# Optimization experiments

Hardware: AMD Instinct MI355X
Metric: run time of the kernel (lower is better)

## Reference

```python
import jax, jax.numpy as jnp
import numpy as np
from jax import lax

B, T, N, D = 64, 2048, 64, 128


def setup_inputs() -> dict:
    key = jax.random.key(0)
    k0, k1, k2, k3, k4 = jax.random.split(key, 5)
    return {
        "X": jax.random.normal(k0, (B, T, D), dtype=jnp.float32),
        "transition_matrix": jax.random.uniform(k1, (N, N), dtype=jnp.float32) / N,
        "state_priors": jax.random.uniform(k2, (N,), dtype=jnp.float32) / N,
        "means": jax.random.normal(k3, (N, D), dtype=jnp.float32),
        "log_vars": jax.random.normal(k4, (N, D), dtype=jnp.float32) * 0.1,
    }


def _emission_logprobs(X, means, log_vars):
    # Diagonal-Gaussian log density per state, vectorized over (B,T,N).
    # sum_d (x-mu)^2 / var expanded into GEMMs to avoid a (B,T,N,D) tensor.
    inv_var = jnp.exp(-log_vars)                               # (N,D)
    t1 = jnp.einsum('btd,nd->btn', X * X, inv_var)             # sum x^2/var
    t2 = jnp.einsum('btd,nd->btn', X, means * inv_var)         # sum x*mu/var
    t3 = jnp.sum(means * means * inv_var + log_vars, axis=-1)  # (N,)
    d = X.shape[-1]
    log2pi = jnp.log(jnp.asarray(2.0 * np.pi, dtype=X.dtype))
    return -0.5 * (t1 - 2.0 * t2 + t3 + d * log2pi)            # (B,T,N)


def reference(X, transition_matrix, state_priors, means, log_vars):
    log_A = jax.nn.log_softmax(transition_matrix, axis=1)      # (N,N)
    log_pi = jax.nn.log_softmax(state_priors, axis=0)          # (N,)
    log_b = _emission_logprobs(X, means, log_vars)             # (B,T,N)

    alpha0 = log_pi + log_b[:, 0]                              # (B,N)
    lb_rest = jnp.moveaxis(log_b[:, 1:], 1, 0)                 # (T-1,B,N)

    def step(alpha_prev, lb_t):
        # alpha_t[j] = log_b_t[j] + logsumexp_i(alpha_{t-1}[i] + log_A[i,j])
        scores = alpha_prev[:, :, None] + log_A[None, :, :]    # (B,N,N)
        alpha_t = lb_t + jax.scipy.special.logsumexp(scores, axis=1)
        return alpha_t, None

    alpha_T, _ = lax.scan(step, alpha0, lb_rest)
    # original gathers log-sum at the last timestep, then sums over subjects
    return jnp.sum(jax.scipy.special.logsumexp(alpha_T, axis=-1))
```

## Files before the change

### kernel.cpp

```cpp
#include <hip/hip_runtime.h>


constexpr int ATF_OFF  = 0;
constexpr int PI_OFF   = 2048;
constexpr int CN_OFF   = 2112;
constexpr int WBF_OFF  = 2176;
constexpr int MV_OFF   = 10368;
constexpr int PART_OFF = 141440;
constexpr int GLS_OFF  = 141504;
constexpr int E_OFF    = 145600;
constexpr int G_OFF    = 4339904;

typedef __attribute__((ext_vector_type(8))) short bf16x8;
typedef __attribute__((ext_vector_type(16))) float f32x16;

union BU { unsigned u[4]; bf16x8 v; };

__device__ inline float wave_max(float v) {
  #pragma unroll
  for (int off = 1; off < 64; off <<= 1) v = fmaxf(v, __shfl_xor(v, off));
  return v;
}
__device__ inline float wave_sum(float v) {
  #pragma unroll
  for (int off = 1; off < 64; off <<= 1) v += __shfl_xor(v, off);
  return v;
}
__device__ inline float read_lane(float v, int l) {
  return __uint_as_float(__builtin_amdgcn_readlane(__float_as_uint(v), l));
}
__device__ inline unsigned f2bf(float f) {
  unsigned u = __float_as_uint(f);
  u += 0x7FFFu + ((u >> 16) & 1u);
  return u >> 16;
}
__device__ inline unsigned cvt_pk(float lo, float hi) {
  unsigned r;
  asm("v_cvt_pk_bf16_f32 %0, %1, %2" : "=v"(r) : "v"(lo), "v"(hi));
  return r;
}

__global__ void setup_kernel(const float* __restrict__ trans,
                             const float* __restrict__ priors,
                             const float* __restrict__ means,
                             const float* __restrict__ log_vars,
                             float* __restrict__ ws) {
  __shared__ float Psh[64 * 64];
  int tid = threadIdx.x, blk = blockIdx.x;

  if (blk == 0) {
    int lane = tid & 63, w = tid >> 6;
    for (int r = 0; r < 16; ++r) {
      int i = w * 16 + r;
      float x = trans[i * 64 + lane];
      float m = wave_max(x);
      float s = wave_sum(__expf(x - m));
      Psh[i * 64 + lane] = __expf(x - (m + __logf(s)));
    }
    if (w == 0) {
      float x = priors[lane];
      float m = wave_max(x);
      float s = wave_sum(__expf(x - m));
      ws[PI_OFF + lane] = __expf(x - (m + __logf(s)));
    }
    __syncthreads();
    for (int idx = tid; idx < 512; idx += 256) {
      int f = idx >> 6, l = idx & 63;
      int I = f >> 2, Kb = f & 3;
      int m = 32 * I + (l & 31);
      int kb = 16 * Kb + 8 * (l >> 5);
      unsigned u[4];
      #pragma unroll
      for (int p = 0; p < 4; ++p) {
        unsigned a = f2bf(Psh[(kb + 2 * p) * 64 + m]);
        unsigned b = f2bf(Psh[(kb + 2 * p + 1) * 64 + m]);
        u[p] = a | (b << 16);
      }
      *reinterpret_cast<uint4*>(&ws[ATF_OFF + idx * 4]) = make_uint4(u[0], u[1], u[2], u[3]);
    }
  } else if (blk <= 8) {
    int idx = (blk - 1) * 256 + tid;
    int f = idx >> 6, l = idx & 63;
    int Kb = f >> 1, J = f & 1;
    int n = 32 * J + (l & 31);
    int kb = 16 * Kb + 8 * (l >> 5);
    unsigned u[4];
    #pragma unroll
    for (int p = 0; p < 4; ++p) {
      int k0 = kb + 2 * p, k1 = k0 + 1;
      int d0 = k0 & 127, d1 = k1 & 127;
      float iv0 = __expf(-log_vars[n * 128 + d0]);
      float iv1 = __expf(-log_vars[n * 128 + d1]);
      float a  = (k0 < 128) ? (-0.5f * iv0) : (means[n * 128 + d0] * iv0);
      float bb = (k1 < 128) ? (-0.5f * iv1) : (means[n * 128 + d1] * iv1);
      u[p] = f2bf(a) | (f2bf(bb) << 16);
    }
    *reinterpret_cast<uint4*>(&ws[WBF_OFF + idx * 4]) = make_uint4(u[0], u[1], u[2], u[3]);
  } else {
    float* part = Psh;
    int n = tid & 63, g = tid >> 6;
    float s = 0.f;
    for (int d = 32 * g; d < 32 * g + 32; ++d) {
      float lv = log_vars[n * 128 + d];
      float mu = means[n * 128 + d];
      s += mu * mu * __expf(-lv) + lv;
    }
    part[g * 64 + n] = s;
    __syncthreads();
    if (tid < 64) {
      float tot = (part[tid] + part[64 + tid]) + (part[128 + tid] + part[192 + tid]);
      ws[CN_OFF + tid] = -0.5f * (tot + 128.0f * 1.8378770664093453f);
    }
  }
}

__global__ __launch_bounds__(256) void emis_kernel(const float* __restrict__ X,
                                                   float* __restrict__ ws) {
  __shared__ uint4 WBs[2048];
  int tid = threadIdx.x;
  const uint4* wbf = reinterpret_cast<const uint4*>(&ws[WBF_OFF]);
  #pragma unroll
  for (int i = 0; i < 8; ++i) WBs[tid + 256 * i] = wbf[tid + 256 * i];

  int lane = tid & 63, w = tid >> 6;
  int il = lane & 31, h = lane >> 5;
  size_t row = (size_t)blockIdx.x * 128 + w * 32 + il;
  const float* Xr = X + row * 128;

  bf16x8 ax[8], asq[8];
  #pragma unroll
  for (int s = 0; s < 8; ++s) {
    float4 v0 = *reinterpret_cast<const float4*>(Xr + s * 16 + 8 * h);
    float4 v1 = *reinterpret_cast<const float4*>(Xr + s * 16 + 8 * h + 4);
    BU bx, bq;
    bx.u[0] = cvt_pk(v0.x, v0.y); bx.u[1] = cvt_pk(v0.z, v0.w);
    bx.u[2] = cvt_pk(v1.x, v1.y); bx.u[3] = cvt_pk(v1.z, v1.w);
    bq.u[0] = cvt_pk(v0.x * v0.x, v0.y * v0.y);
    bq.u[1] = cvt_pk(v0.z * v0.z, v0.w * v0.w);
    bq.u[2] = cvt_pk(v1.x * v1.x, v1.y * v1.y);
    bq.u[3] = cvt_pk(v1.z * v1.z, v1.w * v1.w);
    ax[s] = bx.v; asq[s] = bq.v;
  }
  __syncthreads();

  f32x16 acc0, acc1;
  #pragma unroll
  for (int z = 0; z < 16; ++z) { acc0[z] = 0.f; acc1[z] = 0.f; }
  #pragma unroll
  for (int Kb = 0; Kb < 8; ++Kb) {
    bf16x8 b0 = reinterpret_cast<const BU*>(&WBs[(2 * Kb + 0) * 64 + lane])->v;
    bf16x8 b1 = reinterpret_cast<const BU*>(&WBs[(2 * Kb + 1) * 64 + lane])->v;
    acc0 = __builtin_amdgcn_mfma_f32_32x32x16_bf16(asq[Kb], b0, acc0, 0, 0, 0);
    acc1 = __builtin_amdgcn_mfma_f32_32x32x16_bf16(asq[Kb], b1, acc1, 0, 0, 0);
  }
  #pragma unroll
  for (int Kb = 8; Kb < 16; ++Kb) {
    bf16x8 b0 = reinterpret_cast<const BU*>(&WBs[(2 * Kb + 0) * 64 + lane])->v;
    bf16x8 b1 = reinterpret_cast<const BU*>(&WBs[(2 * Kb + 1) * 64 + lane])->v;
    acc0 = __builtin_amdgcn_mfma_f32_32x32x16_bf16(ax[Kb - 8], b0, acc0, 0, 0, 0);
    acc1 = __builtin_amdgcn_mfma_f32_32x32x16_bf16(ax[Kb - 8], b1, acc1, 0, 0, 0);
  }

  float cn0 = ws[CN_OFF + il];
  float cn1 = ws[CN_OFF + 32 + il];
  unsigned short* Ep = reinterpret_cast<unsigned short*>(&ws[E_OFF]);
  float* MVp = &ws[MV_OFF];
  size_t tbase = (size_t)blockIdx.x * 128 + w * 32;
  #pragma unroll
  for (int e = 0; e < 16; ++e) {
    float v0 = acc0[e] + cn0;
    float v1 = acc1[e] + cn1;
    float mx = fmaxf(v0, v1);
    #pragma unroll
    for (int off = 1; off < 32; off <<= 1) mx = fmaxf(mx, __shfl_xor(mx, off));
    int r = (e & 3) + 8 * (e >> 2) + 4 * h;
    size_t t = tbase + r;
    Ep[t * 64 + il]      = (unsigned short)f2bf(__expf(v0 - mx));
    Ep[t * 64 + 32 + il] = (unsigned short)f2bf(__expf(v1 - mx));
    if (il == 0) MVp[t] = mx;
  }
}

__global__ __launch_bounds__(128, 4) void fwd1_scan(float* __restrict__ ws) {
  const int tid = threadIdx.x;
  const int lane = tid & 63, J = tid >> 6;
  const int h = lane >> 5, il = lane & 31;
  const int job = blockIdx.x, b = job >> 5, cch = job & 31;

  bf16x8 atf0, atf1, atf2, atf3, atf4, atf5, atf6, atf7;
  atf0 = *reinterpret_cast<const bf16x8*>(&ws[ATF_OFF + (0 * 64 + lane) * 4]);
  atf1 = *reinterpret_cast<const bf16x8*>(&ws[ATF_OFF + (1 * 64 + lane) * 4]);
  atf2 = *reinterpret_cast<const bf16x8*>(&ws[ATF_OFF + (2 * 64 + lane) * 4]);
  atf3 = *reinterpret_cast<const bf16x8*>(&ws[ATF_OFF + (3 * 64 + lane) * 4]);
  atf4 = *reinterpret_cast<const bf16x8*>(&ws[ATF_OFF + (4 * 64 + lane) * 4]);
  atf5 = *reinterpret_cast<const bf16x8*>(&ws[ATF_OFF + (5 * 64 + lane) * 4]);
  atf6 = *reinterpret_cast<const bf16x8*>(&ws[ATF_OFF + (6 * 64 + lane) * 4]);
  atf7 = *reinterpret_cast<const bf16x8*>(&ws[ATF_OFF + (7 * 64 + lane) * 4]);

  bf16x8 bf0, bf1, bf2, bf3;
  {
    int js0 = 32 * J + il - 8 * h;
#define IDF(dst, Kb) { int js = js0 - 16 * (Kb); BU bu_;                      \
    _Pragma("unroll")                                                         \
    for (int p = 0; p < 4; ++p)                                               \
      bu_.u[p] = ((js >> 1) == p) ? ((js & 1) ? 0x3F800000u : 0x00003F80u) : 0u; \
    dst = bu_.v; }
    IDF(bf0, 0) IDF(bf1, 1) IDF(bf2, 2) IDF(bf3, 3)
#undef IDF
  }

  const int tstart = 1 + cch * 64;
  const int len = (cch == 31) ? 63 : 64;
  const char* Eb = (const char*)(ws + E_OFF) + ((size_t)b * 2048 + tstart) * 128;

  float Ls = 0.0f;

#define LOADE(dst, idx) {                                                     \
    const char* Ep_ = Eb + (size_t)(idx) * 128;                               \
    _Pragma("unroll")                                                         \
    for (int q_ = 0; q_ < 4; ++q_) {                                          \
      dst[q_]     = *reinterpret_cast<const uint2*>(Ep_ + 16 * q_ + 8 * h);   \
      dst[4 + q_] = *reinterpret_cast<const uint2*>(Ep_ + 64 + 16 * q_ + 8 * h); \
    } }

#define SX(W, z, I)                                                           \
  ({ uint2 u_ = W[4 * (I) + ((z) >> 2)];                                      \
     unsigned w_ = (((z) >> 1) & 1) ? u_.y : u_.x;                            \
     __uint_as_float(((z) & 1) ? (w_ & 0xFFFF0000u) : (w_ << 16)); })

#define BBS(dst, At, p, I, W) {                                               \
    unsigned xe0 = cvt_pk((At)[8*(p)+0] * SX(W, 8*(p)+0, I),                  \
                          (At)[8*(p)+1] * SX(W, 8*(p)+1, I));                 \
    unsigned xe1 = cvt_pk((At)[8*(p)+2] * SX(W, 8*(p)+2, I),                  \
                          (At)[8*(p)+3] * SX(W, 8*(p)+3, I));                 \
    unsigned xo0 = cvt_pk((At)[8*(p)+4] * SX(W, 8*(p)+4, I),                  \
                          (At)[8*(p)+5] * SX(W, 8*(p)+5, I));                 \
    unsigned xo1 = cvt_pk((At)[8*(p)+6] * SX(W, 8*(p)+6, I),                  \
                          (At)[8*(p)+7] * SX(W, 8*(p)+7, I));                 \
    asm("v_permlane32_swap_b32 %0, %1" : "+v"(xe0), "+v"(xo0));               \
    asm("v_permlane32_swap_b32 %0, %1" : "+v"(xe1), "+v"(xo1));               \
    BU bu_; bu_.u[0] = xe0; bu_.u[1] = xe1; bu_.u[2] = xo0; bu_.u[3] = xo1;   \
    dst = bu_.v; }

#define MFMA_HEAD(d, A, B)                                                    \
    asm("v_mfma_f32_32x32x16_bf16 %0, %1, %2, 0"                              \
        : "=&v"(d) : "v"(A), "v"(B));
#define MFMA_ACC(d, A, B)                                                     \
    asm("v_mfma_f32_32x32x16_bf16 %0, %1, %2, %0"                             \
        : "+v"(d) : "v"(A), "v"(B));

#define STEP(EW, DO_RN) {                                                     \
    f32x16 a0, a1;                                                            \
    MFMA_HEAD(a0, atf0, bf0)                                                  \
    MFMA_HEAD(a1, atf4, bf0)                                                  \
    MFMA_ACC(a0, atf1, bf1)                                                   \
    MFMA_ACC(a1, atf5, bf1)                                                   \
    MFMA_ACC(a0, atf2, bf2)                                                   \
    MFMA_ACC(a1, atf6, bf2)                                                   \
    MFMA_ACC(a0, atf3, bf3)                                                   \
    MFMA_ACC(a1, atf7, bf3)                                                   \
    asm volatile("s_nop 7\n\ts_nop 7\n\ts_nop 3" : "+v"(a0), "+v"(a1));       \
    if (DO_RN) {                                                              \
      float mx = 0.f;                                                         \
      _Pragma("unroll")                                                       \
      for (int z = 0; z < 16; ++z) mx = fmaxf(mx, fmaxf(a0[z], a1[z]));       \
      mx = wave_max(mx);                                                      \
      float inv = 1.0f / mx;                                                  \
      Ls += __logf(mx);                                                       \
      _Pragma("unroll")                                                       \
      for (int z = 0; z < 16; ++z) { a0[z] *= inv; a1[z] *= inv; }            \
    }                                                                         \
    BBS(bf0, a0, 0, 0, EW) BBS(bf1, a0, 1, 0, EW)                             \
    BBS(bf2, a1, 0, 1, EW) BBS(bf3, a1, 1, 1, EW) }

  uint2 eA[8];
  #pragma unroll 1
  for (int step = 0; step < len; ++step) {
    LOADE(eA, step);
    STEP(eA, ((step & 7) == 7));
  }

#undef STEP
#undef MFMA_ACC
#undef MFMA_HEAD
#undef BBS
#undef SX
#undef LOADE

  unsigned short* Gb = reinterpret_cast<unsigned short*>(&ws[G_OFF]) + (size_t)job * 4096;
#define GST(fr, Kb) { BU bu_; bu_.v = fr;                                     \
    _Pragma("unroll")                                                         \
    for (int p = 0; p < 4; ++p) {                                             \
      int k = 16 * (Kb) + 8 * h + 2 * p;                                      \
      Gb[k * 64 + 32 * J + il]       = (unsigned short)(bu_.u[p] & 0xFFFFu);  \
      Gb[(k + 1) * 64 + 32 * J + il] = (unsigned short)(bu_.u[p] >> 16);      \
    } }
  GST(bf0, 0) GST(bf1, 1) GST(bf2, 2) GST(bf3, 3)
#undef GST
  if (lane == 0) ws[GLS_OFF + job * 2 + J] = Ls;
}

__global__ __launch_bounds__(64, 1) void fwd2_combine(float* __restrict__ ws) {
  int b = blockIdx.x, j = threadIdx.x;

  float Ms = 0.f;
  for (int k = 0; k < 32; ++k) Ms += ws[MV_OFF + (size_t)b * 2048 + k * 64 + j];
  Ms = wave_sum(Ms);

  const unsigned short* E0 =
      reinterpret_cast<const unsigned short*>(&ws[E_OFF]) + (size_t)b * 2048 * 64;
  float w = ws[PI_OFF + j] * __uint_as_float(((unsigned)E0[j]) << 16);
  float Lacc = Ms;

  const unsigned short* Gb =
      reinterpret_cast<const unsigned short*>(&ws[G_OFF]) + (size_t)b * 32 * 4096;
  for (int c = 0; c < 32; ++c) {
    const uint4* gp = reinterpret_cast<const uint4*>(Gb + (size_t)c * 4096 + j * 64);
    uint4 gw[8];
    #pragma unroll
    for (int s = 0; s < 8; ++s) gw[s] = gp[s];
    float gv[64];
    #pragma unroll
    for (int s = 0; s < 8; ++s) {
      gv[8 * s + 0] = __uint_as_float(gw[s].x << 16);
      gv[8 * s + 1] = __uint_as_float(gw[s].x & 0xFFFF0000u);
      gv[8 * s + 2] = __uint_as_float(gw[s].y << 16);
      gv[8 * s + 3] = __uint_as_float(gw[s].y & 0xFFFF0000u);
      gv[8 * s + 4] = __uint_as_float(gw[s].z << 16);
      gv[8 * s + 5] = __uint_as_float(gw[s].z & 0xFFFF0000u);
      gv[8 * s + 6] = __uint_as_float(gw[s].w << 16);
      gv[8 * s + 7] = __uint_as_float(gw[s].w & 0xFFFF0000u);
    }
    float l0 = 0.f, l1 = 0.f, h0 = 0.f, h1 = 0.f;
    #pragma unroll
    for (int i = 0; i < 32; i += 2) {
      l0 = fmaf(read_lane(w, i + 0), gv[i + 0], l0);
      l1 = fmaf(read_lane(w, i + 1), gv[i + 1], l1);
      h0 = fmaf(read_lane(w, 32 + i + 0), gv[32 + i + 0], h0);
      h1 = fmaf(read_lane(w, 32 + i + 1), gv[32 + i + 1], h1);
    }
    float ylo = l0 + l1, yhi = h0 + h1;
    float g0 = ws[GLS_OFF + (b * 32 + c) * 2 + 0];
    float g1 = ws[GLS_OFF + (b * 32 + c) * 2 + 1];
    float Lm = fmaxf(g0, g1);
    float y = __expf(g0 - Lm) * ylo + __expf(g1 - Lm) * yhi;
    float s = wave_sum(y);
    w = y * (1.0f / s);
    Lacc += Lm + __logf(s);
  }
  float S = wave_sum(w);
  if (j == 0) ws[PART_OFF + b] = Lacc + __logf(S);
}

__global__ void final_kernel(const float* __restrict__ part, float* __restrict__ out) {
  float v = part[threadIdx.x];
  float s = wave_sum(v);
  if (threadIdx.x == 0) out[0] = s;
}

extern "C" void kernel_launch(void* const* d_in, const int* in_sizes, int n_in,
                              void* d_out, int out_size, void* d_ws, size_t ws_size,
                              hipStream_t stream) {
  const float* X        = (const float*)d_in[0];
  const float* trans    = (const float*)d_in[1];
  const float* priors   = (const float*)d_in[2];
  const float* means    = (const float*)d_in[3];
  const float* log_vars = (const float*)d_in[4];
  float* ws  = (float*)d_ws;
  float* out = (float*)d_out;

  hipLaunchKernelGGL(setup_kernel, dim3(10), dim3(256), 0, stream,
                     trans, priors, means, log_vars, ws);
  hipLaunchKernelGGL(emis_kernel, dim3(1024), dim3(256), 0, stream, X, ws);
  hipLaunchKernelGGL(fwd1_scan, dim3(2048), dim3(128), 0, stream, ws);
  hipLaunchKernelGGL(fwd2_combine, dim3(64), dim3(64), 0, stream, ws);
  hipLaunchKernelGGL(final_kernel, dim3(1), dim3(64), 0, stream,
                     ws + PART_OFF, out);
}
```

Measured before the change: 138.7 us.

## Interleave two independent scan chunks per block to hide MFMA latency

Each block of the chunked forward scan now processes two independent time chunks, interleaving their MFMA chains, normalisation and emission loads. The MFMA dependency latency of one chunk can then overlap with the conversion and scaling work of the other. The grid is halved and the occupancy hint drops from 4 to 2 blocks to make room for the doubled register state. The last chunk with 63 steps is handled by clamping the load index and skipping its final finish step.

```diff
diff --git a/kernel.cpp b/kernel.cpp
--- a/kernel.cpp
+++ b/kernel.cpp
@@ -181,11 +181,13 @@
   }
 }
 
-__global__ __launch_bounds__(128, 4) void fwd1_scan(float* __restrict__ ws) {
+__global__ __launch_bounds__(128, 2) void fwd1_scan(float* __restrict__ ws) {
   const int tid = threadIdx.x;
   const int lane = tid & 63, J = tid >> 6;
   const int h = lane >> 5, il = lane & 31;
-  const int job = blockIdx.x, b = job >> 5, cch = job & 31;
+  const int jobA = blockIdx.x * 2, jobB = jobA + 1;
+  const int b = jobA >> 5;
+  const int cchA = jobA & 31, cchB = jobB & 31;
 
   bf16x8 atf0, atf1, atf2, atf3, atf4, atf5, atf6, atf7;
   atf0 = *reinterpret_cast<const bf16x8*>(&ws[ATF_OFF + (0 * 64 + lane) * 4]);
@@ -197,7 +199,7 @@
   atf6 = *reinterpret_cast<const bf16x8*>(&ws[ATF_OFF + (6 * 64 + lane) * 4]);
   atf7 = *reinterpret_cast<const bf16x8*>(&ws[ATF_OFF + (7 * 64 + lane) * 4]);
 
-  bf16x8 bf0, bf1, bf2, bf3;
+  bf16x8 bfA0, bfA1, bfA2, bfA3, bfB0, bfB1, bfB2, bfB3;
   {
     int js0 = 32 * J + il - 8 * h;
 #define IDF(dst, Kb) { int js = js0 - 16 * (Kb); BU bu_;                      \
@@ -205,18 +207,19 @@
     for (int p = 0; p < 4; ++p)                                               \
       bu_.u[p] = ((js >> 1) == p) ? ((js & 1) ? 0x3F800000u : 0x00003F80u) : 0u; \
     dst = bu_.v; }
-    IDF(bf0, 0) IDF(bf1, 1) IDF(bf2, 2) IDF(bf3, 3)
+    IDF(bfA0, 0) IDF(bfA1, 1) IDF(bfA2, 2) IDF(bfA3, 3)
+    IDF(bfB0, 0) IDF(bfB1, 1) IDF(bfB2, 2) IDF(bfB3, 3)
 #undef IDF
   }
 
-  const int tstart = 1 + cch * 64;
-  const int len = (cch == 31) ? 63 : 64;
-  const char* Eb = (const char*)(ws + E_OFF) + ((size_t)b * 2048 + tstart) * 128;
-
-  float Ls = 0.0f;
-
-#define LOADE(dst, idx) {                                                     \
-    const char* Ep_ = Eb + (size_t)(idx) * 128;                               \
+  const int lenB = (cchB == 31) ? 63 : 64;
+  const char* EbA = (const char*)(ws + E_OFF) + ((size_t)b * 2048 + 1 + cchA * 64) * 128;
+  const char* EbB = (const char*)(ws + E_OFF) + ((size_t)b * 2048 + 1 + cchB * 64) * 128;
+
+  float LsA = 0.0f, LsB = 0.0f;
+
+#define LOADE(dst, base, idx) {                                               \
+    const char* Ep_ = (base) + (size_t)(idx) * 128;                           \
     _Pragma("unroll")                                                         \
     for (int q_ = 0; q_ < 4; ++q_) {                                          \
       dst[q_]     = *reinterpret_cast<const uint2*>(Ep_ + 16 * q_ + 8 * h);   \
@@ -249,16 +252,17 @@
     asm("v_mfma_f32_32x32x16_bf16 %0, %1, %2, %0"                             \
         : "+v"(d) : "v"(A), "v"(B));
 
-#define STEP(EW, DO_RN) {                                                     \
-    f32x16 a0, a1;                                                            \
-    MFMA_HEAD(a0, atf0, bf0)                                                  \
-    MFMA_HEAD(a1, atf4, bf0)                                                  \
-    MFMA_ACC(a0, atf1, bf1)                                                   \
-    MFMA_ACC(a1, atf5, bf1)                                                   \
-    MFMA_ACC(a0, atf2, bf2)                                                   \
-    MFMA_ACC(a1, atf6, bf2)                                                   \
-    MFMA_ACC(a0, atf3, bf3)                                                   \
-    MFMA_ACC(a1, atf7, bf3)                                                   \
+#define MFMA8(a0, a1, b0, b1, b2, b3) {                                       \
+    MFMA_HEAD(a0, atf0, b0)                                                   \
+    MFMA_HEAD(a1, atf4, b0)                                                   \
+    MFMA_ACC(a0, atf1, b1)                                                    \
+    MFMA_ACC(a1, atf5, b1)                                                    \
+    MFMA_ACC(a0, atf2, b2)                                                    \
+    MFMA_ACC(a1, atf6, b2)                                                    \
+    MFMA_ACC(a0, atf3, b3)                                                    \
+    MFMA_ACC(a1, atf7, b3) }
+
+#define FINISH(a0, a1, b0, b1, b2, b3, EW, DO_RN, Ls) {                       \
     asm volatile("s_nop 7\n\ts_nop 7\n\ts_nop 3" : "+v"(a0), "+v"(a1));       \
     if (DO_RN) {                                                              \
       float mx = 0.f;                                                         \
@@ -270,24 +274,42 @@
       _Pragma("unroll")                                                       \
       for (int z = 0; z < 16; ++z) { a0[z] *= inv; a1[z] *= inv; }            \
     }                                                                         \
-    BBS(bf0, a0, 0, 0, EW) BBS(bf1, a0, 1, 0, EW)                             \
-    BBS(bf2, a1, 0, 1, EW) BBS(bf3, a1, 1, 1, EW) }
-
-  uint2 eA[8];
+    BBS(b0, a0, 0, 0, EW) BBS(b1, a0, 1, 0, EW)                               \
+    BBS(b2, a1, 0, 1, EW) BBS(b3, a1, 1, 1, EW) }
+
+  uint2 eA[8], eB[8];
+  LOADE(eA, EbA, 0);
+  LOADE(eB, EbB, 0);
+
+  f32x16 aA0, aA1, aB0, aB1;
+  MFMA8(aA0, aA1, bfA0, bfA1, bfA2, bfA3)
+  MFMA8(aB0, aB1, bfB0, bfB1, bfB2, bfB3)
+
   #pragma unroll 1
-  for (int step = 0; step < len; ++step) {
-    LOADE(eA, step);
-    STEP(eA, ((step & 7) == 7));
-  }
-
-#undef STEP
+  for (int s = 0; s < 63; ++s) {
+    bool rn = ((s & 7) == 7);
+    FINISH(aA0, aA1, bfA0, bfA1, bfA2, bfA3, eA, rn, LsA)
+    LOADE(eA, EbA, s + 1)
+    MFMA8(aA0, aA1, bfA0, bfA1, bfA2, bfA3)
+    FINISH(aB0, aB1, bfB0, bfB1, bfB2, bfB3, eB, rn, LsB)
+    LOADE(eB, EbB, (s + 1 < lenB) ? (s + 1) : (lenB - 1))
+    MFMA8(aB0, aB1, bfB0, bfB1, bfB2, bfB3)
+  }
+  FINISH(aA0, aA1, bfA0, bfA1, bfA2, bfA3, eA, true, LsA)
+  if (lenB == 64) {
+    FINISH(aB0, aB1, bfB0, bfB1, bfB2, bfB3, eB, true, LsB)
+  }
+
+#undef FINISH
+#undef MFMA8
 #undef MFMA_ACC
 #undef MFMA_HEAD
 #undef BBS
 #undef SX
 #undef LOADE
 
-  unsigned short* Gb = reinterpret_cast<unsigned short*>(&ws[G_OFF]) + (size_t)job * 4096;
+  {
+    unsigned short* Gb = reinterpret_cast<unsigned short*>(&ws[G_OFF]) + (size_t)jobA * 4096;
 #define GST(fr, Kb) { BU bu_; bu_.v = fr;                                     \
     _Pragma("unroll")                                                         \
     for (int p = 0; p < 4; ++p) {                                             \
@@ -295,9 +317,15 @@
       Gb[k * 64 + 32 * J + il]       = (unsigned short)(bu_.u[p] & 0xFFFFu);  \
       Gb[(k + 1) * 64 + 32 * J + il] = (unsigned short)(bu_.u[p] >> 16);      \
     } }
-  GST(bf0, 0) GST(bf1, 1) GST(bf2, 2) GST(bf3, 3)
+    GST(bfA0, 0) GST(bfA1, 1) GST(bfA2, 2) GST(bfA3, 3)
+    Gb += 4096;
+    GST(bfB0, 0) GST(bfB1, 1) GST(bfB2, 2) GST(bfB3, 3)
 #undef GST
-  if (lane == 0) ws[GLS_OFF + job * 2 + J] = Ls;
+  }
+  if (lane == 0) {
+    ws[GLS_OFF + jobA * 2 + J] = LsA;
+    ws[GLS_OFF + jobB * 2 + J] = LsB;
+  }
 }
 
 __global__ __launch_bounds__(64, 1) void fwd2_combine(float* __restrict__ ws) {
@@ -372,7 +400,7 @@
   hipLaunchKernelGGL(setup_kernel, dim3(10), dim3(256), 0, stream,
                      trans, priors, means, log_vars, ws);
   hipLaunchKernelGGL(emis_kernel, dim3(1024), dim3(256), 0, stream, X, ws);
-  hipLaunchKernelGGL(fwd1_scan, dim3(2048), dim3(128), 0, stream, ws);
+  hipLaunchKernelGGL(fwd1_scan, dim3(1024), dim3(128), 0, stream, ws);
   hipLaunchKernelGGL(fwd2_combine, dim3(64), dim3(64), 0, stream, ws);
   hipLaunchKernelGGL(final_kernel, dim3(1), dim3(64), 0, stream,
                      ws + PART_OFF, out);
```

Result: slower. 145.6 us (+5.0%).

## Fuse emission GEMM into chunked scan kernel, keep emissions in LDS

Applied to the files above, without the earlier changes.

The separate emission kernel goes away. Each scan block now computes the emission probabilities for its own 64-timestep chunk with MFMA and stores them as bf16 in shared memory, so the 16 MB emission tensor no longer round-trips through global memory. The t=0 emission is written to a small fp32 global slot for the combine kernel to read. The combine kernel also prefetches the next chunk's transfer matrix while computing the current one. In exchange, every block reloads the weight fragments from global memory instead of from shared memory, and the GEMM work is spread over 128-thread blocks.

```diff
diff --git a/kernel.cpp b/kernel.cpp
--- a/kernel.cpp
+++ b/kernel.cpp
@@ -8,8 +8,8 @@
 constexpr int MV_OFF   = 10368;
 constexpr int PART_OFF = 141440;
 constexpr int GLS_OFF  = 141504;
-constexpr int E_OFF    = 145600;
-constexpr int G_OFF    = 4339904;
+constexpr int E0G_OFF  = 145600;
+constexpr int G_OFF    = 149696;
 
 typedef __attribute__((ext_vector_type(8))) short bf16x8;
 typedef __attribute__((ext_vector_type(16))) float f32x16;
@@ -114,78 +114,83 @@
   }
 }
 
-__global__ __launch_bounds__(256) void emis_kernel(const float* __restrict__ X,
-                                                   float* __restrict__ ws) {
-  __shared__ uint4 WBs[2048];
-  int tid = threadIdx.x;
-  const uint4* wbf = reinterpret_cast<const uint4*>(&ws[WBF_OFF]);
-  #pragma unroll
-  for (int i = 0; i < 8; ++i) WBs[tid + 256 * i] = wbf[tid + 256 * i];
-
-  int lane = tid & 63, w = tid >> 6;
-  int il = lane & 31, h = lane >> 5;
-  size_t row = (size_t)blockIdx.x * 128 + w * 32 + il;
-  const float* Xr = X + row * 128;
-
-  bf16x8 ax[8], asq[8];
-  #pragma unroll
-  for (int s = 0; s < 8; ++s) {
-    float4 v0 = *reinterpret_cast<const float4*>(Xr + s * 16 + 8 * h);
-    float4 v1 = *reinterpret_cast<const float4*>(Xr + s * 16 + 8 * h + 4);
-    BU bx, bq;
-    bx.u[0] = cvt_pk(v0.x, v0.y); bx.u[1] = cvt_pk(v0.z, v0.w);
-    bx.u[2] = cvt_pk(v1.x, v1.y); bx.u[3] = cvt_pk(v1.z, v1.w);
-    bq.u[0] = cvt_pk(v0.x * v0.x, v0.y * v0.y);
-    bq.u[1] = cvt_pk(v0.z * v0.z, v0.w * v0.w);
-    bq.u[2] = cvt_pk(v1.x * v1.x, v1.y * v1.y);
-    bq.u[3] = cvt_pk(v1.z * v1.z, v1.w * v1.w);
-    ax[s] = bx.v; asq[s] = bq.v;
-  }
-  __syncthreads();
-
-  f32x16 acc0, acc1;
-  #pragma unroll
-  for (int z = 0; z < 16; ++z) { acc0[z] = 0.f; acc1[z] = 0.f; }
-  #pragma unroll
-  for (int Kb = 0; Kb < 8; ++Kb) {
-    bf16x8 b0 = reinterpret_cast<const BU*>(&WBs[(2 * Kb + 0) * 64 + lane])->v;
-    bf16x8 b1 = reinterpret_cast<const BU*>(&WBs[(2 * Kb + 1) * 64 + lane])->v;
-    acc0 = __builtin_amdgcn_mfma_f32_32x32x16_bf16(asq[Kb], b0, acc0, 0, 0, 0);
-    acc1 = __builtin_amdgcn_mfma_f32_32x32x16_bf16(asq[Kb], b1, acc1, 0, 0, 0);
-  }
-  #pragma unroll
-  for (int Kb = 8; Kb < 16; ++Kb) {
-    bf16x8 b0 = reinterpret_cast<const BU*>(&WBs[(2 * Kb + 0) * 64 + lane])->v;
-    bf16x8 b1 = reinterpret_cast<const BU*>(&WBs[(2 * Kb + 1) * 64 + lane])->v;
-    acc0 = __builtin_amdgcn_mfma_f32_32x32x16_bf16(ax[Kb - 8], b0, acc0, 0, 0, 0);
-    acc1 = __builtin_amdgcn_mfma_f32_32x32x16_bf16(ax[Kb - 8], b1, acc1, 0, 0, 0);
-  }
-
-  float cn0 = ws[CN_OFF + il];
-  float cn1 = ws[CN_OFF + 32 + il];
-  unsigned short* Ep = reinterpret_cast<unsigned short*>(&ws[E_OFF]);
-  float* MVp = &ws[MV_OFF];
-  size_t tbase = (size_t)blockIdx.x * 128 + w * 32;
-  #pragma unroll
-  for (int e = 0; e < 16; ++e) {
-    float v0 = acc0[e] + cn0;
-    float v1 = acc1[e] + cn1;
-    float mx = fmaxf(v0, v1);
-    #pragma unroll
-    for (int off = 1; off < 32; off <<= 1) mx = fmaxf(mx, __shfl_xor(mx, off));
-    int r = (e & 3) + 8 * (e >> 2) + 4 * h;
-    size_t t = tbase + r;
-    Ep[t * 64 + il]      = (unsigned short)f2bf(__expf(v0 - mx));
-    Ep[t * 64 + 32 + il] = (unsigned short)f2bf(__expf(v1 - mx));
-    if (il == 0) MVp[t] = mx;
-  }
-}
-
-__global__ __launch_bounds__(128, 4) void fwd1_scan(float* __restrict__ ws) {
+__global__ __launch_bounds__(128, 4) void fused_scan(const float* __restrict__ X,
+                                                     float* __restrict__ ws) {
+  __shared__ __align__(16) unsigned short Esh[64 * 64];
+
   const int tid = threadIdx.x;
   const int lane = tid & 63, J = tid >> 6;
   const int h = lane >> 5, il = lane & 31;
   const int job = blockIdx.x, b = job >> 5, cch = job & 31;
+  const int tstart = 1 + cch * 64;
+  const int len = (cch == 31) ? 63 : 64;
+
+  {
+    int i_lane = J * 32 + il;
+    int t_lane = tstart + i_lane;
+    if (cch == 31 && i_lane == 63) t_lane = 0;
+    const float* Xr = X + ((size_t)b * 2048 + t_lane) * 128;
+
+    bf16x8 ax[8], asq[8];
+    #pragma unroll
+    for (int s = 0; s < 8; ++s) {
+      float4 v0 = *reinterpret_cast<const float4*>(Xr + s * 16 + 8 * h);
+      float4 v1 = *reinterpret_cast<const float4*>(Xr + s * 16 + 8 * h + 4);
+      BU bx, bq;
+      bx.u[0] = cvt_pk(v0.x, v0.y); bx.u[1] = cvt_pk(v0.z, v0.w);
+      bx.u[2] = cvt_pk(v1.x, v1.y); bx.u[3] = cvt_pk(v1.z, v1.w);
+      bq.u[0] = cvt_pk(v0.x * v0.x, v0.y * v0.y);
+      bq.u[1] = cvt_pk(v0.z * v0.z, v0.w * v0.w);
+      bq.u[2] = cvt_pk(v1.x * v1.x, v1.y * v1.y);
+      bq.u[3] = cvt_pk(v1.z * v1.z, v1.w * v1.w);
+      ax[s] = bx.v; asq[s] = bq.v;
+    }
+
+    const uint4* wbf = reinterpret_cast<const uint4*>(&ws[WBF_OFF]);
+    f32x16 acc0, acc1;
+    #pragma unroll
+    for (int z = 0; z < 16; ++z) { acc0[z] = 0.f; acc1[z] = 0.f; }
+    #pragma unroll
+    for (int Kb = 0; Kb < 8; ++Kb) {
+      BU b0, b1;
+      *reinterpret_cast<uint4*>(b0.u) = wbf[(2 * Kb + 0) * 64 + lane];
+      *reinterpret_cast<uint4*>(b1.u) = wbf[(2 * Kb + 1) * 64 + lane];
+      acc0 = __builtin_amdgcn_mfma_f32_32x32x16_bf16(asq[Kb], b0.v, acc0, 0, 0, 0);
+      acc1 = __builtin_amdgcn_mfma_f32_32x32x16_bf16(asq[Kb], b1.v, acc1, 0, 0, 0);
+    }
+    #pragma unroll
+    for (int Kb = 8; Kb < 16; ++Kb) {
+      BU b0, b1;
+      *reinterpret_cast<uint4*>(b0.u) = wbf[(2 * Kb + 0) * 64 + lane];
+      *reinterpret_cast<uint4*>(b1.u) = wbf[(2 * Kb + 1) * 64 + lane];
+      acc0 = __builtin_amdgcn_mfma_f32_32x32x16_bf16(ax[Kb - 8], b0.v, acc0, 0, 0, 0);
+      acc1 = __builtin_amdgcn_mfma_f32_32x32x16_bf16(ax[Kb - 8], b1.v, acc1, 0, 0, 0);
+    }
+
+    float cn0 = ws[CN_OFF + il];
+    float cn1 = ws[CN_OFF + 32 + il];
+    float* MVp = &ws[MV_OFF] + (size_t)b * 2048;
+    #pragma unroll
+    for (int e = 0; e < 16; ++e) {
+      float v0 = acc0[e] + cn0;
+      float v1 = acc1[e] + cn1;
+      float mx = fmaxf(v0, v1);
+      #pragma unroll
+      for (int off = 1; off < 32; off <<= 1) mx = fmaxf(mx, __shfl_xor(mx, off));
+      int r = 32 * J + (e & 3) + 8 * (e >> 2) + 4 * h;
+      float e0 = __expf(v0 - mx), e1 = __expf(v1 - mx);
+      if (cch == 31 && r == 63) {
+        ws[E0G_OFF + b * 64 + il]      = e0;
+        ws[E0G_OFF + b * 64 + 32 + il] = e1;
+        if (il == 0) MVp[0] = mx;
+      } else {
+        Esh[r * 64 + il]      = (unsigned short)f2bf(e0);
+        Esh[r * 64 + 32 + il] = (unsigned short)f2bf(e1);
+        if (il == 0) MVp[tstart + r] = mx;
+      }
+    }
+  }
+  __syncthreads();
 
   bf16x8 atf0, atf1, atf2, atf3, atf4, atf5, atf6, atf7;
   atf0 = *reinterpret_cast<const bf16x8*>(&ws[ATF_OFF + (0 * 64 + lane) * 4]);
@@ -209,14 +214,10 @@
 #undef IDF
   }
 
-  const int tstart = 1 + cch * 64;
-  const int len = (cch == 31) ? 63 : 64;
-  const char* Eb = (const char*)(ws + E_OFF) + ((size_t)b * 2048 + tstart) * 128;
-
   float Ls = 0.0f;
 
 #define LOADE(dst, idx) {                                                     \
-    const char* Ep_ = Eb + (size_t)(idx) * 128;                               \
+    const char* Ep_ = reinterpret_cast<const char*>(Esh) + (size_t)(idx) * 128; \
     _Pragma("unroll")                                                         \
     for (int q_ = 0; q_ < 4; ++q_) {                                          \
       dst[q_]     = *reinterpret_cast<const uint2*>(Ep_ + 16 * q_ + 8 * h);   \
@@ -307,18 +308,23 @@
   for (int k = 0; k < 32; ++k) Ms += ws[MV_OFF + (size_t)b * 2048 + k * 64 + j];
   Ms = wave_sum(Ms);
 
-  const unsigned short* E0 =
-      reinterpret_cast<const unsigned short*>(&ws[E_OFF]) + (size_t)b * 2048 * 64;
-  float w = ws[PI_OFF + j] * __uint_as_float(((unsigned)E0[j]) << 16);
+  float w = ws[PI_OFF + j] * ws[E0G_OFF + b * 64 + j];
   float Lacc = Ms;
 
   const unsigned short* Gb =
       reinterpret_cast<const unsigned short*>(&ws[G_OFF]) + (size_t)b * 32 * 4096;
+  const uint4* gbase = reinterpret_cast<const uint4*>(Gb);
+
+  uint4 gw[8];
+  #pragma unroll
+  for (int s = 0; s < 8; ++s) gw[s] = gbase[j * 4 + s];
+
   for (int c = 0; c < 32; ++c) {
-    const uint4* gp = reinterpret_cast<const uint4*>(Gb + (size_t)c * 4096 + j * 64);
-    uint4 gw[8];
-    #pragma unroll
-    for (int s = 0; s < 8; ++s) gw[s] = gp[s];
+    uint4 gn[8];
+    int cnx = (c + 1 < 32) ? (c + 1) : c;
+    #pragma unroll
+    for (int s = 0; s < 8; ++s) gn[s] = gbase[(size_t)cnx * 256 + j * 4 + s];
+
     float gv[64];
     #pragma unroll
     for (int s = 0; s < 8; ++s) {
@@ -347,6 +353,9 @@
     float s = wave_sum(y);
     w = y * (1.0f / s);
     Lacc += Lm + __logf(s);
+
+    #pragma unroll
+    for (int s2 = 0; s2 < 8; ++s2) gw[s2] = gn[s2];
   }
   float S = wave_sum(w);
   if (j == 0) ws[PART_OFF + b] = Lacc + __logf(S);
@@ -371,8 +380,7 @@
 
   hipLaunchKernelGGL(setup_kernel, dim3(10), dim3(256), 0, stream,
                      trans, priors, means, log_vars, ws);
-  hipLaunchKernelGGL(emis_kernel, dim3(1024), dim3(256), 0, stream, X, ws);
-  hipLaunchKernelGGL(fwd1_scan, dim3(2048), dim3(128), 0, stream, ws);
+  hipLaunchKernelGGL(fused_scan, dim3(2048), dim3(128), 0, stream, X, ws);
   hipLaunchKernelGGL(fwd2_combine, dim3(64), dim3(64), 0, stream, ws);
   hipLaunchKernelGGL(final_kernel, dim3(1), dim3(64), 0, stream,
                      ws + PART_OFF, out);
```

Result: faster. 124.9 us (-10.0%).
